# Kernel optimization log

Hardware: AMD Instinct MI355X
Metric: run time of the kernel (lower is better)

The kernel has to match this reference:

```python
import jax, jax.numpy as jnp
import numpy as np

C = 64   # input_channels
H = 128  # hidden_channels


def setup_inputs() -> dict:
    key = jax.random.key(0)
    ks = jax.random.split(key, 13)
    s = lambda k, shape, fan_in: jax.random.uniform(k, shape, jnp.float32, -1.0, 1.0) / np.sqrt(fan_in)
    return {
        "x": jax.random.normal(ks[0], (2, 512, C), jnp.float32),
        "Wa": s(ks[1], (C, H), C),  "ba": s(ks[2], (H,), C),
        "Wb": s(ks[3], (H, H), H), "bb": s(ks[4], (H,), H),
        "Wc1": s(ks[5], (H, H), H), "bc1": s(ks[6], (H,), H),
        "Wc2": s(ks[7], (H, H), H), "bc2": s(ks[8], (H,), H),
        "Wc3": s(ks[9], (H, H), H), "bc3": s(ks[10], (H,), H),
        "Wo": s(ks[11], (H, 1), H), "bo": s(ks[12], (1,), H),
    }


def reference(x, Wa, ba, Wb, bb, Wc1, bc1, Wc2, bc2, Wc3, bc3, Wo, bo):
    B, N, _ = x.shape
    # node MLP
    h = jax.nn.relu(jnp.einsum("bnc,ch->bnh", x, Wa) + ba)
    h = jax.nn.relu(jnp.einsum("bnh,hk->bnk", h, Wb) + bb)
    # pairwise difference: diff[b,i,j] = h[b,j] - h[b,i]  (matches x_a - x_b)
    d = h[:, None, :, :] - h[:, :, None, :]  # [B,N,N,H]
    e = jax.nn.relu(jnp.einsum("bijh,hk->bijk", d, Wc1) + bc1)
    e = jax.nn.relu(jnp.einsum("bijh,hk->bijk", e, Wc2) + bc2)
    e = jax.nn.relu(jnp.einsum("bijh,hk->bijk", e, Wc3) + bc3)
    out = jnp.einsum("bijh,ho->bijo", e, Wo) + bo  # [B,N,N,1]
    return out[..., 0]  # [B,N,N]
```

## Files before the change

### kernel.cpp

```cpp
#include <hip/hip_runtime.h>


typedef _Float16 half_t;
typedef __attribute__((ext_vector_type(2))) _Float16 f16x2;
typedef __attribute__((ext_vector_type(8))) _Float16 f16x8;
typedef __attribute__((ext_vector_type(4))) float f32x4;


__global__ __launch_bounds__(256) void prep_kernel(
    const float* __restrict__ x, const float* __restrict__ Wa, const float* __restrict__ ba,
    const float* __restrict__ Wb, const float* __restrict__ bb, const float* __restrict__ Wc1,
    const float* __restrict__ bc1, const float* __restrict__ Wc2, const float* __restrict__ Wc3,
    half_t* __restrict__ gh, half_t* __restrict__ gbh,
    half_t* __restrict__ W2T, half_t* __restrict__ W3T)
{
  const int t = threadIdx.x;
  if (blockIdx.x >= 256) {
    const int bid = blockIdx.x - 256;
    const int layer = bid >> 3, nt = bid & 7;
    const int ks = t >> 6, L = t & 63, q = L >> 4, cc = L & 15;
    const float* src = layer ? Wc3 : Wc2;
    half_t* dst = layer ? W3T : W2T;
    f16x8 v;
    #pragma unroll
    for (int e = 0; e < 8; e++)
      v[e] = (half_t)src[(32 * ks + 8 * q + e) * 128 + 16 * nt + cc];
    *(f16x8*)(dst + (nt * 4 + ks) * 512 + L * 8) = v;
    return;
  }
  __shared__ float sx[64 * 6];
  __shared__ float sh1[128 * 6];
  __shared__ float sh2[128 * 6];
  const int n0 = blockIdx.x * 4;
  const int col = t & 127, hf = t >> 7;

  sx[(t & 63) * 6 + (t >> 6)] = x[(n0 + (t >> 6)) * 64 + (t & 63)];
  __syncthreads();

  float a0 = ba[col], a1 = a0;
  #pragma unroll
  for (int cc = 0; cc < 64; cc++) {
    const float wv = Wa[cc * 128 + col];
    const float2 xv = *(const float2*)(sx + cc * 6 + hf * 2);
    a0 = fmaf(xv.x, wv, a0); a1 = fmaf(xv.y, wv, a1);
  }
  *(float2*)(sh1 + col * 6 + hf * 2) = make_float2(fmaxf(a0, 0.f), fmaxf(a1, 0.f));
  __syncthreads();

  float b0 = bb[col], b1 = b0;
  #pragma unroll
  for (int k = 0; k < 128; k++) {
    const float wv = Wb[k * 128 + col];
    const float2 hv = *(const float2*)(sh1 + k * 6 + hf * 2);
    b0 = fmaf(hv.x, wv, b0); b1 = fmaf(hv.y, wv, b1);
  }
  *(float2*)(sh2 + col * 6 + hf * 2) = make_float2(fmaxf(b0, 0.f), fmaxf(b1, 0.f));
  __syncthreads();

  float c0 = 0.f, c1 = 0.f;
  #pragma unroll
  for (int k = 0; k < 128; k++) {
    const float wv = Wc1[k * 128 + col];
    const float2 hv = *(const float2*)(sh2 + k * 6 + hf * 2);
    c0 = fmaf(hv.x, wv, c0); c1 = fmaf(hv.y, wv, c1);
  }
  const float bv = bc1[col];
  const int r0 = n0 + hf * 2;
  gh [(r0 + 0) * 128 + col] = (half_t)c0;
  gh [(r0 + 1) * 128 + col] = (half_t)c1;
  gbh[(r0 + 0) * 128 + col] = (half_t)(c0 + bv);
  gbh[(r0 + 1) * 128 + col] = (half_t)(c1 + bv);
}

static __device__ inline f16x8 relu_sub8(f16x8 a, f16x8 b) {
  f16x8 d = a - b;
  const f16x8 z = {};
  return __builtin_elementwise_max(d, z);
}

__global__ __launch_bounds__(512)
void edge_kernel(
    const half_t* __restrict__ gh, const half_t* __restrict__ gbh,
    const half_t* __restrict__ W2T, const half_t* __restrict__ W3T,
    const float* __restrict__ bc2, const float* __restrict__ bc3,
    const float* __restrict__ Wo, const float* __restrict__ bo,
    float* __restrict__ out)
{
  __shared__ __align__(16) half_t sW2[16384];
  __shared__ __align__(16) half_t sW3[16384];
  __shared__ __align__(16) float  sBf[384];
  __shared__ __align__(16) half_t sE[32768];

  const int t = threadIdx.x, lane = t & 63, w = t >> 6;
  const int c = lane & 15, q = lane >> 4;
  const int bid = blockIdx.x;
  const int b = bid >> 7, jh = (bid >> 6) & 1, ig = bid & 63;
  const int i0 = ig * 8;
  const bool producer = (w < 4);
  const int pw = w & 3;
  const int j0 = jh * 256 + pw * 64;

  #pragma unroll
  for (int k = 0; k < 4; k++) {
    const int off = (k * 512 + t) * 8;
    *(f16x8*)(sW2 + off) = *(const f16x8*)(W2T + off);
    *(f16x8*)(sW3 + off) = *(const f16x8*)(W3T + off);
  }
  if (t < 384) sBf[t] = (t < 128) ? bc2[t] : ((t < 256) ? bc3[t - 128] : Wo[t - 256]);
  __syncthreads();

  const float bo0 = bo[0];
  const int packoff = ((q >> 1) * 16 + c) * 8 + (q & 1) * 4;
  const int rdoff = lane * 8;
  half_t* sEw = sE + pw * 8192;

  #pragma unroll 1
  for (int r = 0; r < 9; ++r) {
    f16x8 be[4][4];
    if (!producer && r >= 1) {
      #pragma unroll
      for (int ks3 = 0; ks3 < 4; ks3++)
        #pragma unroll
        for (int jt = 0; jt < 4; jt++)
          be[ks3][jt] = *(const f16x8*)(sEw + (jt * 4 + ks3) * 512 + rdoff);
    }
    __syncthreads();

    if (producer) {
      if (r < 8) {
        const int i = i0 + r;
        f16x8 e1[4][4];
        {
          f16x8 gih[4];
          #pragma unroll
          for (int ks = 0; ks < 4; ks++)
            gih[ks] = *(const f16x8*)(gh + (size_t)(b * 512 + i) * 128 + ks * 32 + q * 8);
          #pragma unroll
          for (int ks = 0; ks < 4; ks++)
            #pragma unroll
            for (int jt = 0; jt < 4; jt++) {
              const f16x8 gj = *(const f16x8*)(gbh + (size_t)(b * 512 + j0 + jt * 16 + c) * 128 + ks * 32 + q * 8);
              e1[ks][jt] = relu_sub8(gj, gih[ks]);
            }
        }
        #pragma unroll 1
        for (int nt = 0; nt < 8; nt++) {
          f16x8 wf[4];
          #pragma unroll
          for (int ks = 0; ks < 4; ks++)
            wf[ks] = *(const f16x8*)(sW2 + (nt * 4 + ks) * 512 + rdoff);
          const f32x4 b2 = *(const f32x4*)(sBf + nt * 16 + q * 4);
          f32x4 acc[4] = {b2, b2, b2, b2};
          __builtin_amdgcn_s_setprio(1);
          #pragma unroll
          for (int ks = 0; ks < 4; ks++)
            #pragma unroll
            for (int jt = 0; jt < 4; jt++)
              acc[jt] = __builtin_amdgcn_mfma_f32_16x16x32_f16(wf[ks], e1[ks][jt], acc[jt], 0, 0, 0);
          __builtin_amdgcn_s_setprio(0);
          const int po = ((nt >> 1) * 512) + packoff + (nt & 1) * 256;
          #pragma unroll
          for (int jt = 0; jt < 4; jt++) {
            const f32x4 v = acc[jt];
            f16x2 h01, h23;
            h01[0] = (half_t)fmaxf(v[0], 0.f); h01[1] = (half_t)fmaxf(v[1], 0.f);
            h23[0] = (half_t)fmaxf(v[2], 0.f); h23[1] = (half_t)fmaxf(v[3], 0.f);
            uint2 uv;
            uv.x = __builtin_bit_cast(unsigned int, h01);
            uv.y = __builtin_bit_cast(unsigned int, h23);
            *(uint2*)(sEw + jt * 2048 + po) = uv;
          }
        }
      }
    } else {
      if (r >= 1) {
        const int i = i0 + r - 1;
        float p[4] = {0.f, 0.f, 0.f, 0.f};
        #pragma unroll 1
        for (int mt = 0; mt < 8; mt++) {
          f16x8 wf[4];
          #pragma unroll
          for (int ks3 = 0; ks3 < 4; ks3++)
            wf[ks3] = *(const f16x8*)(sW3 + (mt * 4 + ks3) * 512 + rdoff);
          const f32x4 b3 = *(const f32x4*)(sBf + 128 + mt * 16 + q * 4);
          f32x4 acc[4] = {b3, b3, b3, b3};
          __builtin_amdgcn_s_setprio(1);
          #pragma unroll
          for (int ks3 = 0; ks3 < 4; ks3++)
            #pragma unroll
            for (int jt = 0; jt < 4; jt++)
              acc[jt] = __builtin_amdgcn_mfma_f32_16x16x32_f16(wf[ks3], be[ks3][jt], acc[jt], 0, 0, 0);
          __builtin_amdgcn_s_setprio(0);
          const f32x4 wo = *(const f32x4*)(sBf + 256 + mt * 16 + q * 4);
          #pragma unroll
          for (int jt = 0; jt < 4; jt++)
            #pragma unroll
            for (int rr = 0; rr < 4; rr++)
              p[jt] = fmaf(fmaxf(acc[jt][rr], 0.f), wo[rr], p[jt]);
        }
        #pragma unroll
        for (int jt = 0; jt < 4; jt++) {
          p[jt] += __shfl_xor(p[jt], 16, 64);
          p[jt] += __shfl_xor(p[jt], 32, 64);
        }
        if (q == 0) {
          const size_t base = ((size_t)(b * 512 + i)) * 512 + j0;
          #pragma unroll
          for (int jt = 0; jt < 4; jt++)
            out[base + jt * 16 + c] = p[jt] + bo0;
        }
      }
    }
    __syncthreads();
  }
}

extern "C" void kernel_launch(void* const* d_in, const int* in_sizes, int n_in,
                              void* d_out, int out_size, void* d_ws, size_t ws_size,
                              hipStream_t stream)
{
  const float* x   = (const float*)d_in[0];
  const float* Wa  = (const float*)d_in[1];
  const float* ba  = (const float*)d_in[2];
  const float* Wb  = (const float*)d_in[3];
  const float* bb  = (const float*)d_in[4];
  const float* Wc1 = (const float*)d_in[5];
  const float* bc1 = (const float*)d_in[6];
  const float* Wc2 = (const float*)d_in[7];
  const float* bc2 = (const float*)d_in[8];
  const float* Wc3 = (const float*)d_in[9];
  const float* bc3 = (const float*)d_in[10];
  const float* Wo  = (const float*)d_in[11];
  const float* bo  = (const float*)d_in[12];
  float* out = (float*)d_out;

  char* ws = (char*)d_ws;
  half_t* gh  = (half_t*)ws;
  half_t* gbh = (half_t*)(ws + 262144);
  half_t* W2T = (half_t*)(ws + 524288);
  half_t* W3T = (half_t*)(ws + 557056);

  prep_kernel<<<272, 256, 0, stream>>>(x, Wa, ba, Wb, bb, Wc1, bc1, Wc2, Wc3,
                                       gh, gbh, W2T, W3T);
  edge_kernel<<<256, 512, 0, stream>>>(gh, gbh, W2T, W3T, bc2, bc3, Wo, bo, out);
}
```

Before: 128.4 us.

## Replace producer/consumer warp split with per-wave fused layer pipeline

```diff
diff --git a/kernel.cpp b/kernel.cpp
--- a/kernel.cpp
+++ b/kernel.cpp
@@ -87,131 +87,119 @@
     float* __restrict__ out)
 {
   __shared__ __align__(16) half_t sW2[16384];
-  __shared__ __align__(16) half_t sW3[16384];
-  __shared__ __align__(16) float  sBf[384];
-  __shared__ __align__(16) half_t sE[32768];
+  __shared__ __align__(16) half_t sE[8 * 8192];
 
   const int t = threadIdx.x, lane = t & 63, w = t >> 6;
   const int c = lane & 15, q = lane >> 4;
   const int bid = blockIdx.x;
-  const int b = bid >> 7, jh = (bid >> 6) & 1, ig = bid & 63;
-  const int i0 = ig * 8;
-  const bool producer = (w < 4);
-  const int pw = w & 3;
-  const int j0 = jh * 256 + pw * 64;
+  const int b = bid >> 7, ic = bid & 127;
+  const int i0 = ic * 4;
+  const int j0 = w * 64;
 
   #pragma unroll
   for (int k = 0; k < 4; k++) {
     const int off = (k * 512 + t) * 8;
     *(f16x8*)(sW2 + off) = *(const f16x8*)(W2T + off);
-    *(f16x8*)(sW3 + off) = *(const f16x8*)(W3T + off);
-  }
-  if (t < 384) sBf[t] = (t < 128) ? bc2[t] : ((t < 256) ? bc3[t - 128] : Wo[t - 256]);
+  }
   __syncthreads();
 
   const float bo0 = bo[0];
   const int packoff = ((q >> 1) * 16 + c) * 8 + (q & 1) * 4;
   const int rdoff = lane * 8;
-  half_t* sEw = sE + pw * 8192;
+  half_t* sEw = sE + w * 8192;
 
   #pragma unroll 1
-  for (int r = 0; r < 9; ++r) {
-    f16x8 be[4][4];
-    if (!producer && r >= 1) {
+  for (int u = 0; u < 4; u++) {
+    const int i = i0 + u;
+
+    f16x8 e1[4][4];
+    {
+      f16x8 gih[4];
+      #pragma unroll
+      for (int ks = 0; ks < 4; ks++)
+        gih[ks] = *(const f16x8*)(gh + (size_t)(b * 512 + i) * 128 + ks * 32 + q * 8);
+      #pragma unroll
+      for (int ks = 0; ks < 4; ks++)
+        #pragma unroll
+        for (int jt = 0; jt < 4; jt++) {
+          const f16x8 gj = *(const f16x8*)(gbh + (size_t)(b * 512 + j0 + jt * 16 + c) * 128 + ks * 32 + q * 8);
+          e1[ks][jt] = relu_sub8(gj, gih[ks]);
+        }
+    }
+
+    #pragma unroll 1
+    for (int nt = 0; nt < 8; nt++) {
+      f16x8 wf[4];
+      #pragma unroll
+      for (int ks = 0; ks < 4; ks++)
+        wf[ks] = *(const f16x8*)(sW2 + (nt * 4 + ks) * 512 + rdoff);
+      const f32x4 b2 = *(const f32x4*)(bc2 + nt * 16 + q * 4);
+      f32x4 acc[4] = {b2, b2, b2, b2};
+      __builtin_amdgcn_s_setprio(1);
+      #pragma unroll
+      for (int ks = 0; ks < 4; ks++)
+        #pragma unroll
+        for (int jt = 0; jt < 4; jt++)
+          acc[jt] = __builtin_amdgcn_mfma_f32_16x16x32_f16(wf[ks], e1[ks][jt], acc[jt], 0, 0, 0);
+      __builtin_amdgcn_s_setprio(0);
+      const int po = ((nt >> 1) * 512) + packoff + (nt & 1) * 256;
+      #pragma unroll
+      for (int jt = 0; jt < 4; jt++) {
+        const f32x4 v = acc[jt];
+        f16x2 h01, h23;
+        h01[0] = (half_t)fmaxf(v[0], 0.f); h01[1] = (half_t)fmaxf(v[1], 0.f);
+        h23[0] = (half_t)fmaxf(v[2], 0.f); h23[1] = (half_t)fmaxf(v[3], 0.f);
+        uint2 uv;
+        uv.x = __builtin_bit_cast(unsigned int, h01);
+        uv.y = __builtin_bit_cast(unsigned int, h23);
+        *(uint2*)(sEw + jt * 2048 + po) = uv;
+      }
+    }
+
+    {
+      f16x8 be[4][4];
       #pragma unroll
       for (int ks3 = 0; ks3 < 4; ks3++)
         #pragma unroll
         for (int jt = 0; jt < 4; jt++)
           be[ks3][jt] = *(const f16x8*)(sEw + (jt * 4 + ks3) * 512 + rdoff);
-    }
-    __syncthreads();
-
-    if (producer) {
-      if (r < 8) {
-        const int i = i0 + r;
-        f16x8 e1[4][4];
-        {
-          f16x8 gih[4];
-          #pragma unroll
-          for (int ks = 0; ks < 4; ks++)
-            gih[ks] = *(const f16x8*)(gh + (size_t)(b * 512 + i) * 128 + ks * 32 + q * 8);
-          #pragma unroll
-          for (int ks = 0; ks < 4; ks++)
-            #pragma unroll
-            for (int jt = 0; jt < 4; jt++) {
-              const f16x8 gj = *(const f16x8*)(gbh + (size_t)(b * 512 + j0 + jt * 16 + c) * 128 + ks * 32 + q * 8);
-              e1[ks][jt] = relu_sub8(gj, gih[ks]);
-            }
-        }
-        #pragma unroll 1
-        for (int nt = 0; nt < 8; nt++) {
-          f16x8 wf[4];
-          #pragma unroll
-          for (int ks = 0; ks < 4; ks++)
-            wf[ks] = *(const f16x8*)(sW2 + (nt * 4 + ks) * 512 + rdoff);
-          const f32x4 b2 = *(const f32x4*)(sBf + nt * 16 + q * 4);
-          f32x4 acc[4] = {b2, b2, b2, b2};
-          __builtin_amdgcn_s_setprio(1);
-          #pragma unroll
-          for (int ks = 0; ks < 4; ks++)
-            #pragma unroll
-            for (int jt = 0; jt < 4; jt++)
-              acc[jt] = __builtin_amdgcn_mfma_f32_16x16x32_f16(wf[ks], e1[ks][jt], acc[jt], 0, 0, 0);
-          __builtin_amdgcn_s_setprio(0);
-          const int po = ((nt >> 1) * 512) + packoff + (nt & 1) * 256;
-          #pragma unroll
-          for (int jt = 0; jt < 4; jt++) {
-            const f32x4 v = acc[jt];
-            f16x2 h01, h23;
-            h01[0] = (half_t)fmaxf(v[0], 0.f); h01[1] = (half_t)fmaxf(v[1], 0.f);
-            h23[0] = (half_t)fmaxf(v[2], 0.f); h23[1] = (half_t)fmaxf(v[3], 0.f);
-            uint2 uv;
-            uv.x = __builtin_bit_cast(unsigned int, h01);
-            uv.y = __builtin_bit_cast(unsigned int, h23);
-            *(uint2*)(sEw + jt * 2048 + po) = uv;
-          }
-        }
-      }
-    } else {
-      if (r >= 1) {
-        const int i = i0 + r - 1;
-        float p[4] = {0.f, 0.f, 0.f, 0.f};
-        #pragma unroll 1
-        for (int mt = 0; mt < 8; mt++) {
-          f16x8 wf[4];
-          #pragma unroll
-          for (int ks3 = 0; ks3 < 4; ks3++)
-            wf[ks3] = *(const f16x8*)(sW3 + (mt * 4 + ks3) * 512 + rdoff);
-          const f32x4 b3 = *(const f32x4*)(sBf + 128 + mt * 16 + q * 4);
-          f32x4 acc[4] = {b3, b3, b3, b3};
-          __builtin_amdgcn_s_setprio(1);
-          #pragma unroll
-          for (int ks3 = 0; ks3 < 4; ks3++)
-            #pragma unroll
-            for (int jt = 0; jt < 4; jt++)
-              acc[jt] = __builtin_amdgcn_mfma_f32_16x16x32_f16(wf[ks3], be[ks3][jt], acc[jt], 0, 0, 0);
-          __builtin_amdgcn_s_setprio(0);
-          const f32x4 wo = *(const f32x4*)(sBf + 256 + mt * 16 + q * 4);
+
+      float p[4] = {0.f, 0.f, 0.f, 0.f};
+      #pragma unroll 1
+      for (int mt = 0; mt < 8; mt++) {
+        f16x8 wf[4];
+        #pragma unroll
+        for (int ks3 = 0; ks3 < 4; ks3++)
+          wf[ks3] = *(const f16x8*)(W3T + (mt * 4 + ks3) * 512 + rdoff);
+        const f32x4 b3 = *(const f32x4*)(bc3 + mt * 16 + q * 4);
+        f32x4 acc[4] = {b3, b3, b3, b3};
+        __builtin_amdgcn_s_setprio(1);
+        #pragma unroll
+        for (int ks3 = 0; ks3 < 4; ks3++)
           #pragma unroll
           for (int jt = 0; jt < 4; jt++)
-            #pragma unroll
-            for (int rr = 0; rr < 4; rr++)
-              p[jt] = fmaf(fmaxf(acc[jt][rr], 0.f), wo[rr], p[jt]);
-        }
-        #pragma unroll
-        for (int jt = 0; jt < 4; jt++) {
-          p[jt] += __shfl_xor(p[jt], 16, 64);
-          p[jt] += __shfl_xor(p[jt], 32, 64);
-        }
-        if (q == 0) {
-          const size_t base = ((size_t)(b * 512 + i)) * 512 + j0;
+            acc[jt] = __builtin_amdgcn_mfma_f32_16x16x32_f16(wf[ks3], be[ks3][jt], acc[jt], 0, 0, 0);
+        __builtin_amdgcn_s_setprio(0);
+        const f32x4 wo = *(const f32x4*)(Wo + mt * 16 + q * 4);
+        #pragma unroll
+        for (int jt = 0; jt < 4; jt++)
           #pragma unroll
-          for (int jt = 0; jt < 4; jt++)
-            out[base + jt * 16 + c] = p[jt] + bo0;
-        }
+          for (int rr = 0; rr < 4; rr++)
+            p[jt] = fmaf(fmaxf(acc[jt][rr], 0.f), wo[rr], p[jt]);
+      }
+
+      #pragma unroll
+      for (int jt = 0; jt < 4; jt++) {
+        p[jt] += __shfl_xor(p[jt], 16, 64);
+        p[jt] += __shfl_xor(p[jt], 32, 64);
+      }
+      if (q == 0) {
+        const size_t base = ((size_t)(b * 512 + i)) * 512 + j0;
+        #pragma unroll
+        for (int jt = 0; jt < 4; jt++)
+          out[base + jt * 16 + c] = p[jt] + bo0;
       }
     }
-    __syncthreads();
   }
 }
 
```

Result: faster. 122.6 us (-4.5%).
